# Optimization experiments

Hardware: AMD Instinct MI355X
Metric: run time of the kernel (lower is better)

Reference implementation:

```python
import jax, jax.numpy as jnp
import numpy as np

B, D, NR, H = 8, 64, 6, 3        # batch, input_dim, num_relation, num_hop
R2 = 2 * NR                      # relations incl. inverses
NUM_RULE = R2 ** H               # 1728 combinatorial rules
EPS = 1e-6
TAU = 1.0


def _rule_indices():
    # torch.meshgrid (indexing='ij') over num_hop copies of arange(2*NR), stacked on last dim
    a = np.arange(R2)
    grids = np.meshgrid(*([a] * H), indexing="ij")
    return jnp.asarray(np.stack(grids, -1).reshape(-1, H))  # [NUM_RULE, H] int


def setup_inputs() -> dict:
    key = jax.random.key(0)
    ks = jax.random.split(key, 11)
    s = 0.1
    return {
        "query": jax.random.normal(ks[0], (B, D), jnp.float32),
        "relation_emb": jax.random.normal(ks[1], (R2, D), jnp.float32) * s,      # nn.Embedding(2*NR, D)
        "indicator": jax.random.normal(ks[2], (D,), jnp.float32) * s,            # nn.Embedding(1, D)
        "rel_W": jax.random.normal(ks[3], (H, D, R2 * D), jnp.float32) * s,      # per-layer relation_linear
        "rel_b": jax.random.normal(ks[4], (H, R2 * D), jnp.float32) * s,
        "lin_W": jax.random.normal(ks[5], (H, 13 * D, D), jnp.float32) * s,      # per-layer combine Linear(13D->D)
        "lin_b": jax.random.normal(ks[6], (H, D), jnp.float32) * s,
        "mlp_W1": jax.random.normal(ks[7], (2 * D, D), jnp.float32) * s,
        "mlp_b1": jax.random.normal(ks[8], (D,), jnp.float32) * s,
        "mlp_W2": jax.random.normal(ks[9], (D, 1), jnp.float32) * s,
        "mlp_b2": jax.random.normal(ks[10], (1,), jnp.float32) * s,
    }


def reference(query, relation_emb, indicator, rel_W, rel_b, lin_W, lin_b,
              mlp_W1, mlp_b1, mlp_W2, mlp_b2):
    rel_idx = _rule_indices()                       # [R, H]
    Rn = rel_idx.shape[0]

    # PNA degree scales: each graph is a chain; degree_out+1 (boundary self-message)
    # node 0 -> 1 message (boundary only), nodes 1..H -> 2 messages (edge + boundary)
    log_deg_head = jnp.log(jnp.float32(1.0))
    log_deg_tail = jnp.log(jnp.float32(2.0))
    mean_scale = (log_deg_head + H * log_deg_tail) / (H + 1)
    s_head = log_deg_head / mean_scale
    s_tail = log_deg_tail / mean_scale
    scales_head = jnp.stack([jnp.float32(1.0), s_head, 1.0 / jnp.maximum(s_head, 1e-2)])
    scales_tail = jnp.stack([jnp.float32(1.0), s_tail, 1.0 / jnp.maximum(s_tail, 1e-2)])

    # node-0 PNA update: single message == boundary == indicator (constant across graphs)
    # stats layout per feature dim: (mean, max, min, std)
    f0 = jnp.stack([indicator, indicator, indicator,
                    jnp.full((D,), float(np.sqrt(EPS)), indicator.dtype)], -1).reshape(4 * D)
    upd0 = (f0[:, None] * scales_head).reshape(12 * D)

    # boundary / initial hidden: indicator at node 0 of every graph
    hidden = jnp.zeros((B, Rn, H + 1, D), query.dtype)
    hidden = hidden.at[:, :, 0, :].set(indicator)

    for l in range(H):
        # dependent relation table from the query (relation_linear)
        rel_table = (query @ rel_W[l] + rel_b[l]).reshape(B, R2, D)
        rel = rel_table[:, rel_idx]                 # [B, R, H, D] gather per edge
        msg = hidden[:, :, :-1, :] * rel            # distmult message on edges h -> h+1
        # tail-node PNA stats over message set {msg, boundary=0}
        mean = msg * 0.5
        mx = jnp.maximum(msg, 0.0)
        mn = jnp.minimum(msg, 0.0)
        std = jnp.sqrt(jnp.maximum(msg * msg * 0.25, EPS))   # sq_mean - mean^2 = msg^2/4
        feats = jnp.stack([mean, mx, mn, std], -1).reshape(B, Rn, H, 4 * D)
        upd_tail = (feats[..., None] * scales_tail).reshape(B, Rn, H, 12 * D)
        upd = jnp.concatenate(
            [jnp.broadcast_to(upd0, (B, Rn, 1, 12 * D)), upd_tail], axis=2)
        # combine: relu(Linear(cat([input, update])))
        hidden = jax.nn.relu(
            jnp.concatenate([hidden, upd], -1) @ lin_W[l] + lin_b[l])

    # readout at tail node H, concat per-node query
    feat = jnp.concatenate(
        [hidden[:, :, H, :], jnp.broadcast_to(query[:, None, :], (B, Rn, D))], -1)
    score = (jax.nn.relu(feat @ mlp_W1 + mlp_b1) @ mlp_W2 + mlp_b2)[..., 0]   # [B, R]
    attention = jax.nn.softmax(score / TAU, axis=-1)
    r_emb = relation_emb[rel_idx]                   # [R, H, D]
    subgoals = jnp.einsum("br,rhd->bhd", attention, r_emb)
    masks = jnp.ones((B, H), bool)
    return subgoals, masks
```

## Files before the change

kernel.cpp:

```cpp
#include <hip/hip_runtime.h>
#include <hip/hip_bf16.h>


typedef const float* fp;

#define WS_WT     0
#define WS_RELT   49152
#define WS_QW1    67584
#define WS_C2     68096
#define WS_C2W    68160
#define WS_P1     68224
#define WS_Q3     74368
#define WS_Q2     80512
#define WS_QW3    154240
#define WS_SCORES 160384

__device__ __forceinline__ void acc4f(float q, float rv, float4 wv, float& acc){
  float m = q*rv;
  float p = fmaxf(m, 0.f), n = fminf(m, 0.f);
  acc += p*wv.x;
  acc += n*wv.y;
  acc += fmaxf(0.5f*fabsf(m), 1e-3f)*wv.z;
}

__global__ void k_pre1(fp lin_W, fp query, fp rel_W, fp rel_b, fp mlp_W1,
                       fp mlp_b1, float* ws){
  int t = blockIdx.x*256 + threadIdx.x;
  if (t < 49152){
    int c = t & 3; int j = (t>>2)&63; int d = (t>>8)&63; int l = t>>14;
    fp W = lin_W + (size_t)l*832*64 + (64 + 12*d)*64 + j;
    float v = 0.f;
    if (c == 0){
      float w0 = W[0] + (4.f/3.f)*W[64]  + 0.75f*W[128];
      float w1 = W[192] + (4.f/3.f)*W[256] + 0.75f*W[320];
      v = 0.5f*w0 + w1;
    } else if (c == 1){
      float w0 = W[0] + (4.f/3.f)*W[64]  + 0.75f*W[128];
      float w2 = W[384] + (4.f/3.f)*W[448] + 0.75f*W[512];
      v = 0.5f*w0 + w2;
    } else if (c == 2){
      v = W[576] + (4.f/3.f)*W[640] + 0.75f*W[704];
    }
    ws[WS_WT + t] = v;
  } else if (t < 67584){
    int e = t - 49152;
    int d = e & 63; int j = (e>>6)%12; int b = (e/768)&7; int l = e/6144;
    float acc = rel_b[l*768 + j*64 + d];
    fp W = rel_W + (size_t)l*64*768 + j*64 + d;
    fp q = query + b*64;
    #pragma unroll 8
    for (int k=0;k<64;k++) acc += q[k] * W[k*768];
    ws[WS_RELT + e] = acc;
  } else if (t < 68096){
    int e = t - 67584; int b = e>>6; int j = e&63;
    float acc = mlp_b1[j];
    fp q = query + b*64;
    #pragma unroll 8
    for (int i=0;i<64;i++) acc += q[i] * mlp_W1[(64+i)*64 + j];
    ws[WS_QW1 + e] = acc;
  }
}

__global__ void k_pre3(fp indicator, fp lin_W, fp lin_b, float* ws){
  __shared__ float sC2[64], sC2W[64];
  int tid = threadIdx.x;
  if (tid < 64){
    int j = tid;
    float acc = lin_b[j];
    #pragma unroll 8
    for (int d=0; d<64; d++) acc += 1e-3f * ws[WS_WT + ((d<<6)+j)*4 + 2];
    sC2[j] = fmaxf(acc, 0.f);
  }
  __syncthreads();
  if (tid < 64){
    int j = tid;
    float a2 = lin_b[64+j];
    fp W1 = lin_W + 832*64;
    #pragma unroll 8
    for (int k=0;k<64;k++) a2 += sC2[k] * W1[k*64+j];
    sC2W[j] = a2;
    if (blockIdx.x == 0){ ws[WS_C2 + j] = sC2[j]; ws[WS_C2W + j] = a2; }
  }
  __syncthreads();

  int wave = blockIdx.x*4 + (tid>>6);
  int j = tid & 63;
  bool isP = wave < 96;
  int e = isP ? wave : wave - 96;
  int b = e/12, ii = e%12;
  const float4* W4 = (const float4*)(ws + WS_WT + (isP ? 0 : 16384));
  const float* rel = ws + WS_RELT + (isP ? 0 : 6144) + (b*12+ii)*64;
  float acc = isP ? lin_b[j] : sC2W[j];
  #pragma unroll 4
  for (int d=0; d<64; d++){
    float src = isP ? indicator[d] : sC2[d];
    float4 wv = W4[(d<<6)+j];
    acc4f(src, rel[d], wv, acc);
  }
  float* outp = ws + (isP ? WS_P1 : WS_Q3) + e*64 + j;
  *outp = fmaxf(acc, 0.f);
}

__global__ void k_pre4(fp lin_W, fp lin_b, float* ws){
  int wave = blockIdx.x*4 + (threadIdx.x>>6);
  int j = threadIdx.x & 63;
  if (wave < 1152){
    int b = wave/144, i0 = (wave/12)%12, i1 = wave%12;
    const float4* pv   = (const float4*)(ws + WS_P1 + (b*12+i0)*64);
    const float4* relv = (const float4*)(ws + WS_RELT + 6144 + (b*12+i1)*64);
    const float4* W4j  = (const float4*)(ws + WS_WT + 16384) + j;
    float acc = ws[WS_C2W + j];
    #pragma unroll 4
    for (int dc=0; dc<16; dc++){
      float4 rv = relv[dc];
      float4 p  = pv[dc];
      float4 w0 = W4j[(4*dc+0)*64];
      float4 w1 = W4j[(4*dc+1)*64];
      float4 w2 = W4j[(4*dc+2)*64];
      float4 w3 = W4j[(4*dc+3)*64];
      acc4f(p.x, rv.x, w0, acc);
      acc4f(p.y, rv.y, w1, acc);
      acc4f(p.z, rv.z, w2, acc);
      acc4f(p.w, rv.w, w3, acc);
    }
    ws[WS_Q2 + wave*64 + j] = fmaxf(acc, 0.f);
  } else if (wave < 1248){
    int e = wave - 1152;
    const float* q = ws + WS_Q3 + e*64;
    fp W2 = lin_W + 2*832*64;
    float acc = lin_b[128 + j];
    #pragma unroll 8
    for (int k=0;k<64;k++) acc += q[k]*W2[k*64+j];
    ws[WS_QW3 + e*64 + j] = acc;
  }
}

__global__ __launch_bounds__(256, 4) void k_score(fp mlp_W1, fp mlp_W2, float* ws){
  __shared__ float fin[4][4][64];
  int w = threadIdx.x >> 6;
  int j = threadIdx.x & 63;
  int wave = blockIdx.x*4 + w;
  int b = wave/432; int rem = wave%432;
  int i0 = rem/36; int t36 = rem%36;
  int i2 = t36/3;  int i1b = (t36%3)*4;
  const float4* W4j  = (const float4*)(ws + WS_WT + 32768) + j;
  const float4* relv = (const float4*)(ws + WS_RELT + 12288 + (b*12+i2)*64);
  const float* q2base = ws + WS_Q2 + ((b*12+i0)*12 + i1b)*64;
  const float4* q0v = (const float4*)(q2base);
  const float4* q1v = (const float4*)(q2base + 64);
  const float4* q2v = (const float4*)(q2base + 128);
  const float4* q3v = (const float4*)(q2base + 192);
  float a0 = ws[WS_QW3 + (b*12+i2)*64 + j];
  float acc0=a0, acc1=a0, acc2=a0, acc3=a0;
  #pragma unroll 4
  for (int dc=0; dc<16; dc++){
    float4 rv = relv[dc];
    float4 qa = q0v[dc], qb = q1v[dc], qc = q2v[dc], qd = q3v[dc];
    float4 w0 = W4j[(4*dc+0)*64];
    float4 w1 = W4j[(4*dc+1)*64];
    float4 w2 = W4j[(4*dc+2)*64];
    float4 w3 = W4j[(4*dc+3)*64];
    acc4f(qa.x, rv.x, w0, acc0); acc4f(qb.x, rv.x, w0, acc1);
    acc4f(qc.x, rv.x, w0, acc2); acc4f(qd.x, rv.x, w0, acc3);
    acc4f(qa.y, rv.y, w1, acc0); acc4f(qb.y, rv.y, w1, acc1);
    acc4f(qc.y, rv.y, w1, acc2); acc4f(qd.y, rv.y, w1, acc3);
    acc4f(qa.z, rv.z, w2, acc0); acc4f(qb.z, rv.z, w2, acc1);
    acc4f(qc.z, rv.z, w2, acc2); acc4f(qd.z, rv.z, w2, acc3);
    acc4f(qa.w, rv.w, w3, acc0); acc4f(qb.w, rv.w, w3, acc1);
    acc4f(qc.w, rv.w, w3, acc2); acc4f(qd.w, rv.w, w3, acc3);
  }
  fin[w][0][j]=fmaxf(acc0,0.f); fin[w][1][j]=fmaxf(acc1,0.f);
  fin[w][2][j]=fmaxf(acc2,0.f); fin[w][3][j]=fmaxf(acc3,0.f);
  __syncthreads();
  float qw = ws[WS_QW1 + b*64 + j];
  float w2 = mlp_W2[j];
  for (int g=0; g<4; g++){
    float h = qw;
    const float* f = fin[w][g];
    #pragma unroll 8
    for (int i=0;i<64;i++) h += f[i]*mlp_W1[i*64+j];
    h = fmaxf(h, 0.f);
    float s = h * w2;
    for (int off=32; off>0; off>>=1) s += __shfl_down(s, off, 64);
    if (j == 0){
      int r = i0*144 + (i1b+g)*12 + i2;
      ws[WS_SCORES + b*1728 + r] = s;
    }
  }
}

__global__ void k_final(fp relation_emb, float* ws, float* out){
  int b = blockIdx.x, tid = threadIdx.x;
  __shared__ float se[1728];
  __shared__ float red[256];
  __shared__ float bins[36];
  const float* sc = ws + WS_SCORES + b*1728;
  float mx = -1e30f;
  for (int r=tid; r<1728; r+=256){ float v = sc[r]; se[r] = v; mx = fmaxf(mx, v); }
  red[tid] = mx; __syncthreads();
  for (int s=128; s>0; s>>=1){ if (tid<s) red[tid] = fmaxf(red[tid], red[tid+s]); __syncthreads(); }
  mx = red[0]; __syncthreads();
  float ts = 0.f;
  for (int r=tid; r<1728; r+=256){ float e = expf(se[r]-mx); se[r] = e; ts += e; }
  red[tid] = ts; __syncthreads();
  for (int s=128; s>0; s>>=1){ if (tid<s) red[tid] += red[tid+s]; __syncthreads(); }
  float tot = red[0]; __syncthreads();
  if (tid < 36){
    int h = tid/12, jj = tid%12;
    float a = 0.f;
    if (h == 0){
      const float* p = se + jj*144;
      for (int k=0;k<144;k++) a += p[k];
    } else if (h == 1){
      for (int i0=0;i0<12;i0++){
        const float* p = se + i0*144 + jj*12;
        for (int i2=0;i2<12;i2++) a += p[i2];
      }
    } else {
      for (int i0=0;i0<12;i0++)
        for (int i1=0;i1<12;i1++) a += se[i0*144 + i1*12 + jj];
    }
    bins[tid] = a;
  }
  __syncthreads();
  if (tid < 192){
    int h = tid>>6, d = tid&63;
    float acc = 0.f;
    #pragma unroll
    for (int jj=0; jj<12; jj++) acc += bins[h*12+jj] * relation_emb[jj*64+d];
    out[b*192 + tid] = acc/tot;
  }
  if (tid >= 192 && tid < 195){
    out[1536 + b*3 + (tid-192)] = 1.0f;
  }
}

extern "C" void kernel_launch(void* const* d_in, const int* in_sizes, int n_in,
                              void* d_out, int out_size, void* d_ws, size_t ws_size,
                              hipStream_t stream){
  fp query        = (fp)d_in[0];
  fp relation_emb = (fp)d_in[1];
  fp indicator    = (fp)d_in[2];
  fp rel_W        = (fp)d_in[3];
  fp rel_b        = (fp)d_in[4];
  fp lin_W        = (fp)d_in[5];
  fp lin_b        = (fp)d_in[6];
  fp mlp_W1       = (fp)d_in[7];
  fp mlp_b1       = (fp)d_in[8];
  fp mlp_W2       = (fp)d_in[9];
  float* ws = (float*)d_ws;
  float* out = (float*)d_out;

  k_pre1 <<<266, 256, 0, stream>>>(lin_W, query, rel_W, rel_b, mlp_W1, mlp_b1, ws);
  k_pre3 <<<48,  256, 0, stream>>>(indicator, lin_W, lin_b, ws);
  k_pre4 <<<312, 256, 0, stream>>>(lin_W, lin_b, ws);
  k_score<<<864, 256, 0, stream>>>(mlp_W1, mlp_W2, ws);
  k_final<<<8,   256, 0, stream>>>(relation_emb, ws, out);
}
```

Before: 136.8 us.

## Fuse pre3/pre4 into one mid kernel and stage score weights in LDS

Merges the two intermediate kernels into a single 768-thread kernel. Each block recomputes the small C2 and P1 vectors in shared memory instead of round-tripping them through the workspace, which removes one launch and a global dependency. In k_score the layer-3 weight table is staged through shared memory in chunks and the final MLP is interleaved across four accumulators. The cost is redundant C2 computation in every block and extra barriers in k_score.

```diff
diff --git a/kernel.cpp b/kernel.cpp
--- a/kernel.cpp
+++ b/kernel.cpp
@@ -7,13 +7,9 @@
 #define WS_WT     0
 #define WS_RELT   49152
 #define WS_QW1    67584
-#define WS_C2     68096
-#define WS_C2W    68160
-#define WS_P1     68224
-#define WS_Q3     74368
-#define WS_Q2     80512
-#define WS_QW3    154240
-#define WS_SCORES 160384
+#define WS_Q2     68096
+#define WS_QW3    141824
+#define WS_SCORES 142592
 
 __device__ __forceinline__ void acc4f(float q, float rv, float4 wv, float& acc){
   float m = q*rv;
@@ -61,89 +57,65 @@
   }
 }
 
-__global__ void k_pre3(fp indicator, fp lin_W, fp lin_b, float* ws){
-  __shared__ float sC2[64], sC2W[64];
+__global__ void k_mid(fp indicator, fp lin_W, fp lin_b, float* ws){
+  __shared__ float sC2[64], sC2W[64], sP1[64], sQ3[12][64];
   int tid = threadIdx.x;
-  if (tid < 64){
-    int j = tid;
+  int w = tid>>6, j = tid&63;
+  bool isQ2 = blockIdx.x < 96;
+  int b  = isQ2 ? blockIdx.x/12 : blockIdx.x-96;
+  int i0 = isQ2 ? blockIdx.x%12 : 0;
+  if (w == 0){
     float acc = lin_b[j];
     #pragma unroll 8
     for (int d=0; d<64; d++) acc += 1e-3f * ws[WS_WT + ((d<<6)+j)*4 + 2];
     sC2[j] = fmaxf(acc, 0.f);
-  }
-  __syncthreads();
-  if (tid < 64){
-    int j = tid;
+  } else if (w == 1 && isQ2){
+    const float4* W4 = (const float4*)(ws + WS_WT);
+    const float* rel = ws + WS_RELT + (b*12+i0)*64;
+    float acc = lin_b[j];
+    #pragma unroll 4
+    for (int d=0; d<64; d++) acc4f(indicator[d], rel[d], W4[(d<<6)+j], acc);
+    sP1[j] = fmaxf(acc, 0.f);
+  }
+  __syncthreads();
+  if (w == 0){
     float a2 = lin_b[64+j];
     fp W1 = lin_W + 832*64;
     #pragma unroll 8
     for (int k=0;k<64;k++) a2 += sC2[k] * W1[k*64+j];
     sC2W[j] = a2;
-    if (blockIdx.x == 0){ ws[WS_C2 + j] = sC2[j]; ws[WS_C2W + j] = a2; }
-  }
-  __syncthreads();
-
-  int wave = blockIdx.x*4 + (tid>>6);
-  int j = tid & 63;
-  bool isP = wave < 96;
-  int e = isP ? wave : wave - 96;
-  int b = e/12, ii = e%12;
-  const float4* W4 = (const float4*)(ws + WS_WT + (isP ? 0 : 16384));
-  const float* rel = ws + WS_RELT + (isP ? 0 : 6144) + (b*12+ii)*64;
-  float acc = isP ? lin_b[j] : sC2W[j];
-  #pragma unroll 4
-  for (int d=0; d<64; d++){
-    float src = isP ? indicator[d] : sC2[d];
-    float4 wv = W4[(d<<6)+j];
-    acc4f(src, rel[d], wv, acc);
-  }
-  float* outp = ws + (isP ? WS_P1 : WS_Q3) + e*64 + j;
-  *outp = fmaxf(acc, 0.f);
-}
-
-__global__ void k_pre4(fp lin_W, fp lin_b, float* ws){
-  int wave = blockIdx.x*4 + (threadIdx.x>>6);
-  int j = threadIdx.x & 63;
-  if (wave < 1152){
-    int b = wave/144, i0 = (wave/12)%12, i1 = wave%12;
-    const float4* pv   = (const float4*)(ws + WS_P1 + (b*12+i0)*64);
-    const float4* relv = (const float4*)(ws + WS_RELT + 6144 + (b*12+i1)*64);
-    const float4* W4j  = (const float4*)(ws + WS_WT + 16384) + j;
-    float acc = ws[WS_C2W + j];
+  }
+  __syncthreads();
+  const float4* W4 = (const float4*)(ws + WS_WT + 16384);
+  const float* rel = ws + WS_RELT + 6144 + (b*12+w)*64;
+  if (isQ2){
+    float acc = sC2W[j];
     #pragma unroll 4
-    for (int dc=0; dc<16; dc++){
-      float4 rv = relv[dc];
-      float4 p  = pv[dc];
-      float4 w0 = W4j[(4*dc+0)*64];
-      float4 w1 = W4j[(4*dc+1)*64];
-      float4 w2 = W4j[(4*dc+2)*64];
-      float4 w3 = W4j[(4*dc+3)*64];
-      acc4f(p.x, rv.x, w0, acc);
-      acc4f(p.y, rv.y, w1, acc);
-      acc4f(p.z, rv.z, w2, acc);
-      acc4f(p.w, rv.w, w3, acc);
-    }
-    ws[WS_Q2 + wave*64 + j] = fmaxf(acc, 0.f);
-  } else if (wave < 1248){
-    int e = wave - 1152;
-    const float* q = ws + WS_Q3 + e*64;
+    for (int d=0; d<64; d++) acc4f(sP1[d], rel[d], W4[(d<<6)+j], acc);
+    ws[WS_Q2 + ((b*12+i0)*12+w)*64 + j] = fmaxf(acc, 0.f);
+  } else {
+    float acc = sC2W[j];
+    #pragma unroll 4
+    for (int d=0; d<64; d++) acc4f(sC2[d], rel[d], W4[(d<<6)+j], acc);
+    sQ3[w][j] = fmaxf(acc, 0.f);
+    __syncthreads();
     fp W2 = lin_W + 2*832*64;
-    float acc = lin_b[128 + j];
-    #pragma unroll 8
-    for (int k=0;k<64;k++) acc += q[k]*W2[k*64+j];
-    ws[WS_QW3 + e*64 + j] = acc;
-  }
-}
-
-__global__ __launch_bounds__(256, 4) void k_score(fp mlp_W1, fp mlp_W2, float* ws){
+    float a = lin_b[128+j];
+    #pragma unroll 8
+    for (int k=0;k<64;k++) a += sQ3[w][k]*W2[k*64+j];
+    ws[WS_QW3 + (b*12+w)*64 + j] = a;
+  }
+}
+
+__global__ __launch_bounds__(256) void k_score(fp mlp_W1, fp mlp_W2, float* ws){
+  __shared__ float wt_s[4096];
   __shared__ float fin[4][4][64];
-  int w = threadIdx.x >> 6;
-  int j = threadIdx.x & 63;
+  int tid = threadIdx.x, w = tid>>6, j = tid&63;
   int wave = blockIdx.x*4 + w;
-  int b = wave/432; int rem = wave%432;
+  int b = blockIdx.x/108;
+  int rem = wave%432;
   int i0 = rem/36; int t36 = rem%36;
   int i2 = t36/3;  int i1b = (t36%3)*4;
-  const float4* W4j  = (const float4*)(ws + WS_WT + 32768) + j;
   const float4* relv = (const float4*)(ws + WS_RELT + 12288 + (b*12+i2)*64);
   const float* q2base = ws + WS_Q2 + ((b*12+i0)*12 + i1b)*64;
   const float4* q0v = (const float4*)(q2base);
@@ -152,40 +124,57 @@
   const float4* q3v = (const float4*)(q2base + 192);
   float a0 = ws[WS_QW3 + (b*12+i2)*64 + j];
   float acc0=a0, acc1=a0, acc2=a0, acc3=a0;
-  #pragma unroll 4
-  for (int dc=0; dc<16; dc++){
-    float4 rv = relv[dc];
-    float4 qa = q0v[dc], qb = q1v[dc], qc = q2v[dc], qd = q3v[dc];
-    float4 w0 = W4j[(4*dc+0)*64];
-    float4 w1 = W4j[(4*dc+1)*64];
-    float4 w2 = W4j[(4*dc+2)*64];
-    float4 w3 = W4j[(4*dc+3)*64];
-    acc4f(qa.x, rv.x, w0, acc0); acc4f(qb.x, rv.x, w0, acc1);
-    acc4f(qc.x, rv.x, w0, acc2); acc4f(qd.x, rv.x, w0, acc3);
-    acc4f(qa.y, rv.y, w1, acc0); acc4f(qb.y, rv.y, w1, acc1);
-    acc4f(qc.y, rv.y, w1, acc2); acc4f(qd.y, rv.y, w1, acc3);
-    acc4f(qa.z, rv.z, w2, acc0); acc4f(qb.z, rv.z, w2, acc1);
-    acc4f(qc.z, rv.z, w2, acc2); acc4f(qd.z, rv.z, w2, acc3);
-    acc4f(qa.w, rv.w, w3, acc0); acc4f(qb.w, rv.w, w3, acc1);
-    acc4f(qc.w, rv.w, w3, acc2); acc4f(qd.w, rv.w, w3, acc3);
-  }
+  const float4* Wt2 = (const float4*)(ws + WS_WT + 32768);
+  for (int ch=0; ch<4; ch++){
+    __syncthreads();
+    {
+      const float4* src = Wt2 + ch*1024;
+      float4* dst = (float4*)wt_s;
+      #pragma unroll
+      for (int k=0; k<4; k++) dst[tid + k*256] = src[tid + k*256];
+    }
+    __syncthreads();
+    #pragma unroll
+    for (int dq=0; dq<4; dq++){
+      int dc = ch*4 + dq;
+      float4 rv = relv[dc];
+      float4 qa = q0v[dc], qb = q1v[dc], qc = q2v[dc], qd = q3v[dc];
+      const float4* wl = (const float4*)wt_s + dq*256 + j;
+      float4 w0 = wl[0], w1 = wl[64], w2 = wl[128], w3 = wl[192];
+      acc4f(qa.x, rv.x, w0, acc0); acc4f(qb.x, rv.x, w0, acc1);
+      acc4f(qc.x, rv.x, w0, acc2); acc4f(qd.x, rv.x, w0, acc3);
+      acc4f(qa.y, rv.y, w1, acc0); acc4f(qb.y, rv.y, w1, acc1);
+      acc4f(qc.y, rv.y, w1, acc2); acc4f(qd.y, rv.y, w1, acc3);
+      acc4f(qa.z, rv.z, w2, acc0); acc4f(qb.z, rv.z, w2, acc1);
+      acc4f(qc.z, rv.z, w2, acc2); acc4f(qd.z, rv.z, w2, acc3);
+      acc4f(qa.w, rv.w, w3, acc0); acc4f(qb.w, rv.w, w3, acc1);
+      acc4f(qc.w, rv.w, w3, acc2); acc4f(qd.w, rv.w, w3, acc3);
+    }
+  }
+  __syncthreads();
   fin[w][0][j]=fmaxf(acc0,0.f); fin[w][1][j]=fmaxf(acc1,0.f);
   fin[w][2][j]=fmaxf(acc2,0.f); fin[w][3][j]=fmaxf(acc3,0.f);
   __syncthreads();
   float qw = ws[WS_QW1 + b*64 + j];
-  float w2 = mlp_W2[j];
-  for (int g=0; g<4; g++){
-    float h = qw;
-    const float* f = fin[w][g];
-    #pragma unroll 8
-    for (int i=0;i<64;i++) h += f[i]*mlp_W1[i*64+j];
-    h = fmaxf(h, 0.f);
-    float s = h * w2;
-    for (int off=32; off>0; off>>=1) s += __shfl_down(s, off, 64);
-    if (j == 0){
-      int r = i0*144 + (i1b+g)*12 + i2;
-      ws[WS_SCORES + b*1728 + r] = s;
-    }
+  float w2v = mlp_W2[j];
+  float h0=qw, h1=qw, h2=qw, h3=qw;
+  #pragma unroll 8
+  for (int i=0;i<64;i++){
+    float wv = mlp_W1[i*64+j];
+    h0 += fin[w][0][i]*wv; h1 += fin[w][1][i]*wv;
+    h2 += fin[w][2][i]*wv; h3 += fin[w][3][i]*wv;
+  }
+  float s0=fmaxf(h0,0.f)*w2v, s1=fmaxf(h1,0.f)*w2v;
+  float s2=fmaxf(h2,0.f)*w2v, s3=fmaxf(h3,0.f)*w2v;
+  #pragma unroll
+  for (int off=32; off>0; off>>=1){
+    s0 += __shfl_down(s0, off, 64); s1 += __shfl_down(s1, off, 64);
+    s2 += __shfl_down(s2, off, 64); s3 += __shfl_down(s3, off, 64);
+  }
+  if (j == 0){
+    int rbase = i0*144 + i1b*12 + i2;
+    float* S = ws + WS_SCORES + b*1728 + rbase;
+    S[0] = s0; S[12] = s1; S[24] = s2; S[36] = s3;
   }
 }
 
@@ -252,8 +241,7 @@
   float* out = (float*)d_out;
 
   k_pre1 <<<266, 256, 0, stream>>>(lin_W, query, rel_W, rel_b, mlp_W1, mlp_b1, ws);
-  k_pre3 <<<48,  256, 0, stream>>>(indicator, lin_W, lin_b, ws);
-  k_pre4 <<<312, 256, 0, stream>>>(lin_W, lin_b, ws);
+  k_mid  <<<104, 768, 0, stream>>>(indicator, lin_W, lin_b, ws);
   k_score<<<864, 256, 0, stream>>>(mlp_W1, mlp_W2, ws);
   k_final<<<8,   256, 0, stream>>>(relation_emb, ws, out);
 }
```

Result: faster. 124.8 us (-8.8%).
